# Performance work log

Measured on AMD Instinct MI355X. Metric: run time of the kernel, lower is better.

## Reference

```python
import jax, jax.numpy as jnp
import numpy as np

DMODEL = 1024

def setup_inputs() -> dict:
    key = jax.random.key(0)
    ks = jax.random.split(key, 7)
    scale = 1.0 / np.sqrt(DMODEL)
    x = jax.random.normal(ks[0], (4, 2048, DMODEL), dtype=jnp.float32)
    Wq = jax.random.normal(ks[1], (DMODEL, DMODEL), dtype=jnp.float32) * scale
    bq = jnp.zeros((DMODEL,), dtype=jnp.float32)
    Wk = jax.random.normal(ks[2], (DMODEL, DMODEL), dtype=jnp.float32) * scale
    bk = jnp.zeros((DMODEL,), dtype=jnp.float32)
    Wv = jax.random.normal(ks[3], (DMODEL, DMODEL), dtype=jnp.float32) * scale
    bv = jnp.zeros((DMODEL,), dtype=jnp.float32)
    return {"x": x, "Wq": Wq, "bq": bq, "Wk": Wk, "bk": bk, "Wv": Wv, "bv": bv}

def reference(x, Wq, bq, Wk, bk, Wv, bv):
    # QKV projections: [b, s, d]
    q = jnp.einsum('bsd,de->bse', x, Wq) + bq
    k = jnp.einsum('bsd,de->bse', x, Wk) + bk
    v = jnp.einsum('bsd,de->bse', x, Wv) + bv
    # scaled dot-product attention, full [b, s, s] score matrix (as in source)
    scores = jnp.einsum('bqd,bkd->bqk', q, k) / jnp.sqrt(jnp.asarray(q.shape[-1], q.dtype))
    weights = jax.nn.softmax(scores, axis=-1)
    return jnp.einsum('bqk,bkd->bqd', weights, v)
```

## Files before the change

### kernel.cpp

```cpp
#include <hip/hip_runtime.h>

typedef unsigned short u16;
typedef __attribute__((ext_vector_type(8))) short short8;
typedef __attribute__((ext_vector_type(4))) short short4v;
typedef __attribute__((ext_vector_type(4))) float f32x4;


__device__ __forceinline__ u16 f2bf(float f) {
  union { float f; unsigned u; } c; c.f = f;
  unsigned u = c.u;
  unsigned r = u + 0x7fffu + ((u >> 16) & 1u);
  return (u16)(r >> 16);
}

__device__ __forceinline__ float bf2f(u16 b) {
  union { unsigned u; float f; } c; c.u = ((unsigned)b) << 16;
  return c.f;
}

__device__ __forceinline__ void load_lds16(const void* g, void* l) {
  __builtin_amdgcn_global_load_lds(
      (__attribute__((address_space(1))) void*)(__UINTPTR_TYPE__)(g),
      (__attribute__((address_space(3))) void*)(l),
      16, 0, 0);
}

template <int N> __device__ __forceinline__ void vm_wait() {
  if constexpr (N == 0) asm volatile("s_waitcnt vmcnt(0)");
  else if constexpr (N == 3) asm volatile("s_waitcnt vmcnt(3)");
  else if constexpr (N == 4) asm volatile("s_waitcnt vmcnt(4)");
}

template <int BM, int MODE>
__global__ __launch_bounds__(512)
void gemm256(const u16* __restrict__ A, const u16* __restrict__ Bt,
             void* __restrict__ C0, void* __restrict__ C1,
             const float* __restrict__ b0, const float* __restrict__ b1,
             const float* __restrict__ b2,
             int K, int lda, int ldb, int ldc, float scale,
             long zsA, long zsB, long zsC)
{
  constexpr int MREP = BM / 32;
  constexpr int LA   = BM / 128;
  constexpr int BOFF = BM * 64;
  constexpr int LDSE = BM * 64 + 16384;
  __shared__ __align__(16) u16 lds[2][LDSE];

  A  += (long)blockIdx.z * zsA;
  Bt += (long)blockIdx.z * zsB;

  int bxi, byi;
  if (MODE == 3) {
    const int gw   = gridDim.x;
    const int nwg  = gw * gridDim.y;
    const int orig = blockIdx.x + gw * blockIdx.y;
    const int s    = (orig & 7) * (nwg >> 3) + (orig >> 3);
    bxi = s % gw; byi = s / gw;
  } else {
    bxi = blockIdx.x; byi = blockIdx.y;
  }

  const int t    = threadIdx.x;
  const int lane = t & 63;
  const int wave = t >> 6;
  const int wr   = wave >> 2;
  const int wc   = wave & 3;
  const long brow = (long)byi * BM;
  const long bcol = (long)bxi * 256;

  f32x4 acc[MREP][4];
#pragma unroll
  for (int m = 0; m < MREP; ++m)
#pragma unroll
    for (int n = 0; n < 4; ++n)
#pragma unroll
      for (int j = 0; j < 4; ++j) acc[m][n][j] = 0.f;

  const int frA  = wr * (BM / 2) + (lane & 15);
  const int kAsw = (((lane >> 4) ^ ((frA >> 1) & 3)) * 8);
  const int frB  = wc * 64 + (lane & 15);
  const int kBsw = (((lane >> 4) ^ ((frB >> 1) & 3)) * 8);

  const int sr  = t >> 2;
  const int ssl = ((t & 3) ^ ((sr >> 1) & 3)) * 8;
  const u16* gA = A  + (size_t)(brow + sr) * lda + ssl;
  const u16* gB = Bt + (size_t)(bcol + sr) * ldb + ssl;
  const int NT = K >> 6;

#define STAGE_A(nb, kt1, ks) do {                                   \
    u16* d = &lds[(nb)][(ks) * (BM * 32) + t * 8];                  \
    const u16* g = gA + (size_t)(kt1) * 64 + (ks) * 32;             \
    load_lds16(g, d);                                               \
    if (LA == 2) load_lds16(g + (size_t)128 * lda, d + 4096);       \
  } while (0)

#define STAGE_B(nb, kt1, ks) do {                                   \
    u16* d = &lds[(nb)][BOFF + (ks) * 8192 + t * 8];                \
    const u16* g = gB + (size_t)(kt1) * 64 + (ks) * 32;             \
    load_lds16(g, d);                                               \
    load_lds16(g + (size_t)128 * ldb, d + 4096);                    \
  } while (0)

#define PHASE2(ks, STG, VM) {                                                    \
    _Pragma("unroll")                                                            \
    for (int i = 0; i < MREP; ++i)                                               \
      af[i] = *(const short8*)&bufA[(ks) * (BM * 32) +                           \
                 (size_t)(frA + i * 16) * 32 + kAsw];                            \
    _Pragma("unroll")                                                            \
    for (int n = 0; n < 4; ++n)                                                  \
      bf[n] = *(const short8*)&bufB[(ks) * 8192 +                                \
                 (size_t)(frB + n * 16) * 32 + kBsw];                            \
    STG;                                                                         \
    __builtin_amdgcn_s_barrier();                                                \
    asm volatile("s_waitcnt lgkmcnt(0)");                                        \
    __builtin_amdgcn_s_setprio(1);                                               \
    _Pragma("unroll")                                                            \
    for (int i = 0; i < MREP; ++i)                                               \
      _Pragma("unroll")                                                          \
      for (int n = 0; n < 4; ++n)                                                \
        acc[i][n] = __builtin_amdgcn_mfma_f32_16x16x32_bf16(                     \
            af[i], bf[n], acc[i][n], 0, 0, 0);                                   \
    __builtin_amdgcn_s_setprio(0);                                               \
    VM;                                                                          \
    __builtin_amdgcn_s_barrier();                                                \
  }

  STAGE_A(0, 0, 0); STAGE_B(0, 0, 0); STAGE_A(0, 0, 1); STAGE_B(0, 0, 1);
  vm_wait<0>();
  __builtin_amdgcn_s_barrier();

  short8 af[MREP], bf[4];
  for (int kt = 0; kt < NT - 1; ++kt) {
    const u16* bufA = &lds[kt & 1][0];
    const u16* bufB = bufA + BOFF;
    const int nb = (kt + 1) & 1;
    PHASE2(0, { STAGE_A(nb, kt + 1, 0); STAGE_B(nb, kt + 1, 0); }, vm_wait<LA + 2>())
    PHASE2(1, { STAGE_A(nb, kt + 1, 1); STAGE_B(nb, kt + 1, 1); }, vm_wait<LA + 2>())
  }
  {
    const u16* bufA = &lds[(NT - 1) & 1][0];
    const u16* bufB = bufA + BOFF;
    PHASE2(0, (void)0, vm_wait<0>())
    PHASE2(1, (void)0, (void)0)
  }
#undef PHASE2
#undef STAGE_A
#undef STAGE_B

  const int dcol = lane & 15;
  const int dr4  = (lane >> 4) * 4;
  if (MODE == 3) {
    constexpr int SMSK = BM / 4 - 1;
    u16* sm = (u16*)lds;
#pragma unroll
    for (int m = 0; m < MREP; ++m) {
#pragma unroll
      for (int n = 0; n < 4; ++n) {
        const int cpl = wc * 64 + n * 16 + dcol;
        const int r0l = wr * (BM / 2) + m * 16 + dr4;
        const float bias = b2 ? b2[bcol + cpl] : 0.f;
        short4v w;
#pragma unroll
        for (int j = 0; j < 4; ++j)
          w[j] = (short)f2bf((acc[m][n][j] + bias) * scale);
        *(short4v*)&sm[cpl * BM + (((r0l >> 2) ^ (cpl & SMSK)) << 2)] = w;
      }
    }
    __syncthreads();
    u16* dst = (u16*)C1;
#pragma unroll
    for (int it = 0; it < BM / 16; ++it) {
      const int idx = it * 512 + t;
      const int i  = idx / (BM / 8);
      const int ch = idx & (BM / 8 - 1);
      const short4v lo = *(const short4v*)&sm[i * BM + ((((ch * 2)    ) ^ (i & SMSK)) << 2)];
      const short4v hi = *(const short4v*)&sm[i * BM + ((((ch * 2) + 1) ^ (i & SMSK)) << 2)];
      short8 o;
      o[0] = lo[0]; o[1] = lo[1]; o[2] = lo[2]; o[3] = lo[3];
      o[4] = hi[0]; o[5] = hi[1]; o[6] = hi[2]; o[7] = hi[3];
      *(short8*)&dst[(size_t)(bcol + i) * ldc + brow + ch * 8] = o;
    }
  } else if (MODE == 5) {
    const float* ug = b0 + (long)blockIdx.z * 2048;
    const float* vg = b1 + (long)blockIdx.z * 2048;
    const float c0v = b2[0];
    float* part = (float*)C1 + ((long)blockIdx.z * 32 + (bxi * 4 + wc)) * 2048;
    u16* dst = (u16*)C0 + (long)blockIdx.z * zsC;
#pragma unroll
    for (int m = 0; m < MREP; ++m) {
      const long row0 = brow + wr * (BM / 2) + m * 16 + dr4;
      float uval[4];
#pragma unroll
      for (int j = 0; j < 4; ++j) uval[j] = ug[row0 + j] + c0v;
      float rv[4] = {0.f, 0.f, 0.f, 0.f};
#pragma unroll
      for (int n = 0; n < 4; ++n) {
        const long col = bcol + wc * 64 + n * 16 + dcol;
        const float vv = vg[col];
#pragma unroll
        for (int j = 0; j < 4; ++j) {
          const float p = __expf(acc[m][n][j] + uval[j] + vv);
          dst[(row0 + j) * ldc + col] = f2bf(p);
          rv[j] += p;
        }
      }
#pragma unroll
      for (int j = 0; j < 4; ++j) {
#pragma unroll
        for (int o = 1; o < 16; o <<= 1) rv[j] += __shfl_xor(rv[j], o);
      }
      if (dcol == 0) {
#pragma unroll
        for (int j = 0; j < 4; ++j) part[row0 + j] = rv[j];
      }
    }
  } else if (MODE == 6) {
    const float* part = (const float*)C1 + (long)blockIdx.z * 32 * 2048;
    float* smf = (float*)lds;
    {
      const int r = t >> 2, q4 = t & 3;
      float s = 0.f;
#pragma unroll
      for (int i = 0; i < 8; ++i) s += part[(q4 * 8 + i) * 2048 + brow + r];
      smf[r * 4 + q4] = s;
    }
    __syncthreads();
    if (t < 128)
      smf[512 + t] = 1.0f / (smf[4 * t] + smf[4 * t + 1] + smf[4 * t + 2] + smf[4 * t + 3]);
    __syncthreads();
#pragma unroll
    for (int m = 0; m < MREP; ++m) {
      const long row0 = brow + wr * (BM / 2) + m * 16 + dr4;
      const int  rl   = (int)(row0 - brow);
      float inv[4];
#pragma unroll
      for (int j = 0; j < 4; ++j) inv[j] = smf[512 + rl + j];
#pragma unroll
      for (int n = 0; n < 4; ++n) {
        const long col = bcol + wc * 64 + n * 16 + dcol;
#pragma unroll
        for (int j = 0; j < 4; ++j)
          ((float*)C0)[(long)blockIdx.z * zsC + (row0 + j) * ldc + col] =
              acc[m][n][j] * inv[j];
      }
    }
  } else {
#pragma unroll
    for (int m = 0; m < MREP; ++m) {
#pragma unroll
      for (int n = 0; n < 4; ++n) {
        const long col  = bcol + wc * 64 + n * 16 + dcol;
        const long row0 = brow + wr * (BM / 2) + m * 16 + dr4;
        if (MODE == 1) {
#pragma unroll
          for (int j = 0; j < 4; ++j)
            ((u16*)C0)[(long)blockIdx.z * zsC + (row0 + j) * ldc + col] =
                f2bf(acc[m][n][j] * scale);
        } else {
#pragma unroll
          for (int j = 0; j < 4; ++j)
            ((float*)C0)[(long)blockIdx.z * zsC + (row0 + j) * ldc + col] =
                acc[m][n][j];
        }
      }
    }
  }
}

__global__ __launch_bounds__(256)
void cvt_bf16(const float* __restrict__ in, u16* __restrict__ out, int n4)
{
  int i = blockIdx.x * 256 + threadIdx.x;
  const int stride = gridDim.x * 256;
  for (; i < n4; i += stride) {
    const float4 f = ((const float4*)in)[i];
    ushort4 u;
    u.x = f2bf(f.x); u.y = f2bf(f.y); u.z = f2bf(f.z); u.w = f2bf(f.w);
    ((ushort4*)out)[i] = u;
  }
}

__global__ __launch_bounds__(256)
void wtrans(const float* __restrict__ W, u16* __restrict__ Wt)
{
  __shared__ u16 tile[32][33];
  const int tx = threadIdx.x;
  const int ty = threadIdx.y;
  const int bx = blockIdx.x * 32;
  const int by = blockIdx.y * 32;
#pragma unroll
  for (int i = 0; i < 4; ++i)
    tile[ty + i * 8][tx] = f2bf(W[(size_t)(by + ty + i * 8) * 1024 + bx + tx]);
  __syncthreads();
#pragma unroll
  for (int i = 0; i < 4; ++i)
    Wt[(size_t)(bx + ty + i * 8) * 1024 + by + tx] = tile[tx][ty + i * 8];
}

__global__ __launch_bounds__(256)
void bias_w(const float* __restrict__ Wq, const float* __restrict__ Wk,
            const float* __restrict__ bq, const float* __restrict__ bk,
            float* __restrict__ w1, float* __restrict__ w2,
            float* __restrict__ c0, float qs)
{
  const int wave = threadIdx.x >> 6, lane = threadIdx.x & 63;
  const int row = blockIdx.x * 4 + wave;
  const float* mat = (row < 1024) ? (Wq + (size_t)row * 1024)
                                  : (Wk + (size_t)(row - 1024) * 1024);
  const float* bv = (row < 1024) ? bk : bq;
  float s = 0.f;
#pragma unroll
  for (int i = 0; i < 4; ++i) {
    const float4 mv = *(const float4*)&mat[lane * 4 + i * 256];
    const float4 bb = *(const float4*)&bv[lane * 4 + i * 256];
    s += mv.x * bb.x + mv.y * bb.y + mv.z * bb.z + mv.w * bb.w;
  }
#pragma unroll
  for (int o = 32; o; o >>= 1) s += __shfl_xor(s, o);
  if (lane == 0) ((row < 1024) ? w1 : w2)[row & 1023] = s * qs;
  if (blockIdx.x == 0 && wave == 0) {
    float c = 0.f;
#pragma unroll
    for (int i = 0; i < 4; ++i) {
      const float4 a = *(const float4*)&bq[lane * 4 + i * 256];
      const float4 b = *(const float4*)&bk[lane * 4 + i * 256];
      c += a.x * b.x + a.y * b.y + a.z * b.z + a.w * b.w;
    }
#pragma unroll
    for (int o = 32; o; o >>= 1) c += __shfl_xor(c, o);
    if (lane == 0) c0[0] = c * qs;
  }
}

__global__ __launch_bounds__(256)
void uv_vec(const u16* __restrict__ xb, const float* __restrict__ w1,
            const float* __restrict__ w2, float* __restrict__ u,
            float* __restrict__ v)
{
  const int wave = threadIdx.x >> 6, lane = threadIdx.x & 63;
  const long row = (long)blockIdx.x * 4 + wave;
  const u16* xr = xb + row * 1024;
  float su = 0.f, sv = 0.f;
#pragma unroll
  for (int h = 0; h < 2; ++h) {
    const int d0 = lane * 8 + h * 512;
    const short8 xv = *(const short8*)&xr[d0];
#pragma unroll
    for (int k = 0; k < 8; ++k) {
      const float xf = bf2f((u16)xv[k]);
      su += xf * w1[d0 + k];
      sv += xf * w2[d0 + k];
    }
  }
#pragma unroll
  for (int o = 32; o; o >>= 1) { su += __shfl_xor(su, o); sv += __shfl_xor(sv, o); }
  if (lane == 0) { u[row] = su; v[row] = sv; }
}

extern "C" void kernel_launch(void* const* d_in, const int* in_sizes, int n_in,
                              void* d_out, int out_size, void* d_ws, size_t ws_size,
                              hipStream_t stream)
{
  const float* x  = (const float*)d_in[0];
  const float* Wq = (const float*)d_in[1];
  const float* bq = (const float*)d_in[2];
  const float* Wk = (const float*)d_in[3];
  const float* bk = (const float*)d_in[4];
  const float* Wv = (const float*)d_in[5];
  const float* bv = (const float*)d_in[6];
  float* out = (float*)d_out;
  char* ws = (char*)d_ws;

  const size_t MB = (size_t)1 << 20;
  const float qscale = 0.03125f;
  const long  SO = 2048L * 1024;

  u16* T    = (u16*)(ws);
  u16* xb   = (u16*)(ws + 16 * MB);
  u16* Vt   = (u16*)(ws + 32 * MB);
  u16* Sc   = (u16*)(ws + 48 * MB);
  u16* Wqb  = (u16*)(ws + 80 * MB);
  u16* Wkb  = (u16*)(ws + 82 * MB);
  u16* Wvt  = (u16*)(ws + 84 * MB);
  u16* Mt   = (u16*)(ws + 86 * MB);
  float* partial = (float*)(ws + 88 * MB);
  float* uvec    = (float*)(ws + 89 * MB);
  float* vvec    = (float*)(ws + 89 * MB + 32768);
  float* c0p     = (float*)(ws + 89 * MB + 65536);

  cvt_bf16<<<2048, 256, 0, stream>>>(x, xb, (4 * 2048 * 1024) / 4);
  cvt_bf16<<<512, 256, 0, stream>>>(Wq, Wqb, (1024 * 1024) / 4);
  cvt_bf16<<<512, 256, 0, stream>>>(Wk, Wkb, (1024 * 1024) / 4);
  {
    dim3 tb(32, 8), tg(32, 32);
    wtrans<<<tg, tb, 0, stream>>>(Wv, Wvt);
  }
  bias_w<<<512, 256, 0, stream>>>(Wq, Wk, bq, bk, uvec, vvec, c0p, qscale);

  gemm256<128, 3><<<dim3(4, 8), 512, 0, stream>>>(
      Wqb, Wkb, nullptr, Mt, nullptr, nullptr, nullptr,
      1024, 1024, 1024, 1024, qscale, 0, 0, 0);

  gemm256<128, 3><<<dim3(4, 64), 512, 0, stream>>>(
      xb, Wvt, nullptr, Vt, nullptr, nullptr, bv,
      1024, 1024, 1024, 8192, 1.0f, 0, 0, 0);

  bias_w<<<512, 256, 0, stream>>>(Wq, Wk, bq, bk, partial, partial + 1024, c0p, qscale);
  uv_vec<<<2048, 256, 0, stream>>>(xb, partial, partial + 1024, uvec, vvec);

  gemm256<256, 1><<<dim3(4, 32), 512, 0, stream>>>(
      xb, Mt, T, nullptr, nullptr, nullptr, nullptr,
      1024, 1024, 1024, 1024, 1.0f, 0, 0, 0);

  gemm256<256, 5><<<dim3(8, 8, 4), 512, 0, stream>>>(
      T, xb, Sc, partial, uvec, vvec, c0p,
      1024, 1024, 1024, 2048, 1.0f, SO, SO, 2048L * 2048);

  gemm256<128, 6><<<dim3(4, 16, 4), 512, 0, stream>>>(
      Sc, Vt, out, partial, nullptr, nullptr, nullptr,
      2048, 2048, 8192, 1024, 1.0f, 2048L * 2048, 2048, SO);
}
```

Measured before the change: 190.4 us.

## Accumulate softmax row sums atomically and swizzle all GEMM tile orders

The exp-score GEMM now adds its per-row partial sums straight into a zeroed global rowsum buffer with atomics. The normalising PV GEMM therefore reads the row sums directly instead of reducing 32 partials through LDS with two barriers. The block-index swizzle now applies to every GEMM mode, not only mode 3. The x·Mt GEMM uses a smaller 128-row tile with twice as many blocks, and the redundant second bias_w call is removed. This adds a memset and float-atomic contention, and makes the row sums depend on accumulation order.

Measured after the change: 181.0 us. -4.9%, faster.

```diff
diff --git a/kernel.cpp b/kernel.cpp
--- a/kernel.cpp
+++ b/kernel.cpp
@@ -50,14 +50,12 @@
   Bt += (long)blockIdx.z * zsB;
 
   int bxi, byi;
-  if (MODE == 3) {
+  {
     const int gw   = gridDim.x;
     const int nwg  = gw * gridDim.y;
     const int orig = blockIdx.x + gw * blockIdx.y;
     const int s    = (orig & 7) * (nwg >> 3) + (orig >> 3);
     bxi = s % gw; byi = s / gw;
-  } else {
-    bxi = blockIdx.x; byi = blockIdx.y;
   }
 
   const int t    = threadIdx.x;
@@ -184,7 +182,7 @@
     const float* ug = b0 + (long)blockIdx.z * 2048;
     const float* vg = b1 + (long)blockIdx.z * 2048;
     const float c0v = b2[0];
-    float* part = (float*)C1 + ((long)blockIdx.z * 32 + (bxi * 4 + wc)) * 2048;
+    float* rs = (float*)C1 + (long)blockIdx.z * 2048;
     u16* dst = (u16*)C0 + (long)blockIdx.z * zsC;
 #pragma unroll
     for (int m = 0; m < MREP; ++m) {
@@ -211,30 +209,17 @@
       }
       if (dcol == 0) {
 #pragma unroll
-        for (int j = 0; j < 4; ++j) part[row0 + j] = rv[j];
+        for (int j = 0; j < 4; ++j) atomicAdd(&rs[row0 + j], rv[j]);
       }
     }
   } else if (MODE == 6) {
-    const float* part = (const float*)C1 + (long)blockIdx.z * 32 * 2048;
-    float* smf = (float*)lds;
-    {
-      const int r = t >> 2, q4 = t & 3;
-      float s = 0.f;
-#pragma unroll
-      for (int i = 0; i < 8; ++i) s += part[(q4 * 8 + i) * 2048 + brow + r];
-      smf[r * 4 + q4] = s;
-    }
-    __syncthreads();
-    if (t < 128)
-      smf[512 + t] = 1.0f / (smf[4 * t] + smf[4 * t + 1] + smf[4 * t + 2] + smf[4 * t + 3]);
-    __syncthreads();
+    const float* rs = (const float*)C1 + (long)blockIdx.z * 2048;
 #pragma unroll
     for (int m = 0; m < MREP; ++m) {
       const long row0 = brow + wr * (BM / 2) + m * 16 + dr4;
-      const int  rl   = (int)(row0 - brow);
       float inv[4];
 #pragma unroll
-      for (int j = 0; j < 4; ++j) inv[j] = smf[512 + rl + j];
+      for (int j = 0; j < 4; ++j) inv[j] = 1.0f / rs[row0 + j];
 #pragma unroll
       for (int n = 0; n < 4; ++n) {
         const long col = bcol + wc * 64 + n * 16 + dcol;
@@ -383,10 +368,13 @@
   u16* Wkb  = (u16*)(ws + 82 * MB);
   u16* Wvt  = (u16*)(ws + 84 * MB);
   u16* Mt   = (u16*)(ws + 86 * MB);
-  float* partial = (float*)(ws + 88 * MB);
-  float* uvec    = (float*)(ws + 89 * MB);
-  float* vvec    = (float*)(ws + 89 * MB + 32768);
-  float* c0p     = (float*)(ws + 89 * MB + 65536);
+  char* base88 = ws + 88 * MB;
+  float* w1     = (float*)(base88);
+  float* w2     = (float*)(base88 + 4096);
+  float* uvec   = (float*)(base88 + 8192);
+  float* vvec   = (float*)(base88 + 8192 + 32768);
+  float* c0p    = (float*)(base88 + 8192 + 65536);
+  float* rowsum = (float*)(base88 + 8192 + 65536 + 4096);
 
   cvt_bf16<<<2048, 256, 0, stream>>>(x, xb, (4 * 2048 * 1024) / 4);
   cvt_bf16<<<512, 256, 0, stream>>>(Wq, Wqb, (1024 * 1024) / 4);
@@ -395,7 +383,8 @@
     dim3 tb(32, 8), tg(32, 32);
     wtrans<<<tg, tb, 0, stream>>>(Wv, Wvt);
   }
-  bias_w<<<512, 256, 0, stream>>>(Wq, Wk, bq, bk, uvec, vvec, c0p, qscale);
+  bias_w<<<512, 256, 0, stream>>>(Wq, Wk, bq, bk, w1, w2, c0p, qscale);
+  uv_vec<<<2048, 256, 0, stream>>>(xb, w1, w2, uvec, vvec);
 
   gemm256<128, 3><<<dim3(4, 8), 512, 0, stream>>>(
       Wqb, Wkb, nullptr, Mt, nullptr, nullptr, nullptr,
@@ -405,18 +394,17 @@
       xb, Wvt, nullptr, Vt, nullptr, nullptr, bv,
       1024, 1024, 1024, 8192, 1.0f, 0, 0, 0);
 
-  bias_w<<<512, 256, 0, stream>>>(Wq, Wk, bq, bk, partial, partial + 1024, c0p, qscale);
-  uv_vec<<<2048, 256, 0, stream>>>(xb, partial, partial + 1024, uvec, vvec);
-
-  gemm256<256, 1><<<dim3(4, 32), 512, 0, stream>>>(
+  hipMemsetAsync(rowsum, 0, 4 * 2048 * sizeof(float), stream);
+
+  gemm256<128, 1><<<dim3(4, 64), 512, 0, stream>>>(
       xb, Mt, T, nullptr, nullptr, nullptr, nullptr,
       1024, 1024, 1024, 1024, 1.0f, 0, 0, 0);
 
   gemm256<256, 5><<<dim3(8, 8, 4), 512, 0, stream>>>(
-      T, xb, Sc, partial, uvec, vvec, c0p,
+      T, xb, Sc, rowsum, uvec, vvec, c0p,
       1024, 1024, 1024, 2048, 1.0f, SO, SO, 2048L * 2048);
 
   gemm256<128, 6><<<dim3(4, 16, 4), 512, 0, stream>>>(
-      Sc, Vt, out, partial, nullptr, nullptr, nullptr,
+      Sc, Vt, out, rowsum, nullptr, nullptr, nullptr,
       2048, 2048, 8192, 1024, 1.0f, 2048L * 2048, 2048, SO);
 }
```
